# Kernel tuning notes

Measured on AMD Instinct MI355X. Metric: run time of the kernel, lower is better.

Reference implementation:

```python
import jax, jax.numpy as jnp
import numpy as np

EMBED_DIM = 256
NUM_HEADS = 8
HEAD_DIM = EMBED_DIM // NUM_HEADS


def setup_inputs() -> dict:
    key = jax.random.key(0)
    ks = jax.random.split(key, 6)
    B, Nq, Nkv, C = 2, 4096, 4096, EMBED_DIM
    s = 0.02
    return {
        "query": jax.random.normal(ks[0], (B, Nq, C), dtype=jnp.float32),
        "key_value": jax.random.normal(ks[1], (B, Nkv, C), dtype=jnp.float32),
        "w_q": jax.random.normal(ks[2], (C, C), dtype=jnp.float32) * s,
        "w_kv": jax.random.normal(ks[3], (C, 2 * C), dtype=jnp.float32) * s,
        "w_out": jax.random.normal(ks[4], (C, C), dtype=jnp.float32) * s,
        "b_out": jax.random.normal(ks[5], (C,), dtype=jnp.float32) * s,
    }


def reference(query, key_value, w_q, w_kv, w_out, b_out):
    B, Nq, C = query.shape
    Nkv = key_value.shape[1]
    H, D = NUM_HEADS, HEAD_DIM
    scale = D ** -0.5
    # projections (Linear with no bias for q/kv)
    q = (query @ w_q).reshape(B, Nq, H, D).transpose(0, 2, 1, 3)       # [B,H,Nq,D]
    kv = (key_value @ w_kv).reshape(B, Nkv, 2, H, D)
    kv = kv.transpose(2, 0, 3, 1, 4)                                    # [2,B,H,Nkv,D]
    k, v = kv[0], kv[1]
    # full score matrix, as in the original (dropout = eval-mode identity)
    attn = jnp.einsum("bhqd,bhkd->bhqk", q, k) * scale                  # [B,H,Nq,Nkv]
    attn = jax.nn.softmax(attn, axis=-1)
    out = jnp.einsum("bhqk,bhkd->bhqd", attn, v)                        # [B,H,Nq,D]
    out = out.transpose(0, 2, 1, 3).reshape(B, Nq, C)
    return out @ w_out + b_out
```

## Files before the change

kernel.cpp:

```cpp
#include <hip/hip_runtime.h>

typedef __attribute__((ext_vector_type(8))) short bf16x8;
typedef __attribute__((ext_vector_type(4))) float f32x4;
typedef __attribute__((ext_vector_type(16))) float f32x16;

#define NQ   4096
#define NKV  4096
#define CDIM 256
#define HEADS 8
#define DDIM 32
#define APAD 264

__device__ __forceinline__ unsigned short f2bf(float x){
  unsigned int u = __builtin_bit_cast(unsigned int, x);
  u = (u + 0x7FFFu + ((u >> 16) & 1u)) >> 16;
  return (unsigned short)u;
}

__device__ __forceinline__ float bf2f_lo(unsigned int u){
  return __builtin_bit_cast(float, u << 16);
}
__device__ __forceinline__ float bf2f_hi(unsigned int u){
  return __builtin_bit_cast(float, u & 0xFFFF0000u);
}

__global__ __launch_bounds__(256) void prep_w(
    const float* __restrict__ wq, const float* __restrict__ wkv,
    const float* __restrict__ wout,
    unsigned short* __restrict__ wqT, unsigned short* __restrict__ wkvT,
    unsigned short* __restrict__ woutT)
{
  int i = blockIdx.x * 256 + threadIdx.x;
  if (i < 65536){ int n = i >> 8, k = i & 255; wqT[i] = f2bf(wq[k*256 + n]); }
  else if (i < 196608){ int j = i - 65536; int n = j >> 8, k = j & 255;
                        wkvT[j] = f2bf(wkv[k*512 + n]); }
  else { int j = i - 196608; int n = j >> 8, k = j & 255;
         woutT[j] = f2bf(wout[k*256 + n]); }
}

__global__ __launch_bounds__(256) void gemm_qkv(
    const float* __restrict__ qf,
    const float* __restrict__ kvf,
    const unsigned short* __restrict__ wqT,
    const unsigned short* __restrict__ wkvT,
    unsigned short* __restrict__ QT,
    unsigned short* __restrict__ Kb,
    unsigned short* __restrict__ VTb)
{
  __shared__ unsigned short alds[64 * APAD];
  const int tid = threadIdx.x;
  const int wid = tid >> 6;
  const int lane = tid & 63;
  const int l15 = lane & 15, g = lane >> 4;
  const int m0 = blockIdx.x * 64;
  const int mode = blockIdx.y >= 4;
  const int ny = mode ? (blockIdx.y - 4) : blockIdx.y;
  const int n0 = ny * 64 + wid * 16;
  const float* Xf = mode ? kvf : qf;
  const unsigned short* WT = mode ? wkvT : wqT;

  #pragma unroll
  for (int it = 0; it < 8; ++it){
    int c = it * 256 + tid;
    int row = c >> 5, col = (c & 31) * 8;
    const float4* src = (const float4*)(Xf + (size_t)(m0 + row) * CDIM + col);
    float4 a = src[0], b = src[1];
    union { unsigned short u[8]; bf16x8 v; } o;
    o.u[0]=f2bf(a.x); o.u[1]=f2bf(a.y); o.u[2]=f2bf(a.z); o.u[3]=f2bf(a.w);
    o.u[4]=f2bf(b.x); o.u[5]=f2bf(b.y); o.u[6]=f2bf(b.z); o.u[7]=f2bf(b.w);
    *(bf16x8*)(&alds[row * APAD + col]) = o.v;
  }
  __syncthreads();

  f32x4 acc[4] = {{0,0,0,0},{0,0,0,0},{0,0,0,0},{0,0,0,0}};
  const unsigned short* wp = WT + (size_t)(n0 + l15) * CDIM + g * 8;
  #pragma unroll
  for (int k0 = 0; k0 < CDIM; k0 += 32){
    bf16x8 bfr = *(const bf16x8*)(wp + k0);
    #pragma unroll
    for (int i = 0; i < 4; ++i){
      bf16x8 afr = *(const bf16x8*)(&alds[(l15 + i*16) * APAD + k0 + g*8]);
      acc[i] = __builtin_amdgcn_mfma_f32_16x16x32_bf16(afr, bfr, acc[i], 0, 0, 0);
    }
  }
  const int n = n0 + l15;
  const int b = m0 >> 12;
  const int pos0b = (m0 & 4095) + g * 4;
  if (!mode){
    const int h = n >> 5, d = n & 31;
    const size_t rowbase = ((size_t)(b*HEADS + h)*DDIM + d) * NQ;
    #pragma unroll
    for (int i = 0; i < 4; ++i){
      unsigned int p0 = f2bf(acc[i][0] * 0.25503227f);
      unsigned int p1 = f2bf(acc[i][1] * 0.25503227f);
      unsigned int p2 = f2bf(acc[i][2] * 0.25503227f);
      unsigned int p3 = f2bf(acc[i][3] * 0.25503227f);
      *(uint2*)(&QT[rowbase + pos0b + i*16]) = make_uint2(p0 | (p1<<16), p2 | (p3<<16));
    }
  } else if (n < 256){
    const int h = n >> 5, d = n & 31;
    #pragma unroll
    for (int i = 0; i < 4; ++i){
      #pragma unroll
      for (int r = 0; r < 4; ++r){
        Kb[((size_t)(b*HEADS + h)*NKV + (pos0b + i*16 + r))*DDIM + d] = f2bf(acc[i][r]);
      }
    }
  } else {
    const int c = n - 256, h = c >> 5, d = c & 31;
    const size_t rowbase = ((size_t)(b*HEADS + h)*DDIM + d) * NKV;
    #pragma unroll
    for (int i = 0; i < 4; ++i){
      unsigned int p0 = f2bf(acc[i][0]);
      unsigned int p1 = f2bf(acc[i][1]);
      unsigned int p2 = f2bf(acc[i][2]);
      unsigned int p3 = f2bf(acc[i][3]);
      *(uint2*)(&VTb[rowbase + pos0b + i*16]) = make_uint2(p0 | (p1<<16), p2 | (p3<<16));
    }
  }
}

__global__ __launch_bounds__(256) void gemm_out(
    const unsigned short* __restrict__ AO2,
    const unsigned short* __restrict__ WT,
    float* __restrict__ FO,
    const float* __restrict__ bias)
{
  const int wid = threadIdx.x >> 6;
  const int lane = threadIdx.x & 63;
  const int l15 = lane & 15, g = lane >> 4;
  const int m0 = blockIdx.x * 64;
  const int n0 = blockIdx.y * 64 + wid * 16;
  const int base_b = m0 >> 12, pos0 = m0 & 4095;
  f32x4 acc[4] = {{0,0,0,0},{0,0,0,0},{0,0,0,0},{0,0,0,0}};
  const unsigned short* wp = WT + (size_t)(n0 + l15) * CDIM + g * 8;
  #pragma unroll
  for (int k0 = 0; k0 < CDIM; k0 += 32){
    bf16x8 bfr = *(const bf16x8*)(wp + k0);
    const int h = k0 >> 5;
    const unsigned short* xp = AO2
        + ((size_t)(base_b*HEADS + h)*NQ + pos0 + l15)*DDIM + g*8;
    #pragma unroll
    for (int i = 0; i < 4; ++i){
      bf16x8 afr = *(const bf16x8*)(xp + (size_t)i*16*DDIM);
      acc[i] = __builtin_amdgcn_mfma_f32_16x16x32_bf16(afr, bfr, acc[i], 0, 0, 0);
    }
  }
  #pragma unroll
  for (int i = 0; i < 4; ++i){
    #pragma unroll
    for (int r = 0; r < 4; ++r){
      int m = m0 + i*16 + g*4 + r;
      int n = n0 + l15;
      FO[(size_t)m*CDIM + n] = acc[i][r] + bias[n];
    }
  }
}

template<int NSPLIT>
__global__ __launch_bounds__(512, 4) void attn15(
    const unsigned short* __restrict__ QT,
    const unsigned short* __restrict__ Kb,
    const unsigned short* __restrict__ VT,
    unsigned short* __restrict__ P0, unsigned short* __restrict__ P1,
    unsigned short* __restrict__ P2, unsigned short* __restrict__ P3,
    float* __restrict__ ml)
{
  constexpr int NPHASE = 4096 / NSPLIT / 64;
  __shared__ unsigned short lk[4][2048];
  __shared__ unsigned short lv[4][2048];
  const int wid = threadIdx.x >> 6;
  const int lane = threadIdx.x & 63;
  const int l31 = lane & 31, g1 = lane >> 5;
  const int lin = blockIdx.x;
  const int xcd = lin & 7;
  const int j = lin >> 3;
  const int qg = j & 15;
  const int rest = j >> 4;
  const int kvpart = rest & (NSPLIT - 1);
  const int bh = xcd + 8 * (rest / NSPLIT);
  const int q0w = qg * 256 + wid * 32;
  const int kvoff = kvpart * (NPHASE * 64);

  const unsigned short* QTp = QT + (size_t)bh * DDIM * NQ;
  const unsigned short* KpH = Kb + ((size_t)bh * NKV + kvoff) * DDIM;
  const unsigned short* VpH = VT + (size_t)bh * DDIM * NKV + kvoff;

  union { unsigned short u[8]; bf16x8 v; } qa, qb;
  #pragma unroll
  for (int d = 0; d < 8; ++d)
    qa.u[d] = QTp[(size_t)(8*g1 + d) * NQ + q0w + l31];
  #pragma unroll
  for (int d = 0; d < 8; ++d)
    qb.u[d] = QTp[(size_t)(16 + 8*g1 + d) * NQ + q0w + l31];
  const bf16x8 qf0 = qa.v, qf1 = qb.v;

  union { unsigned short u[8]; bf16x8 v; } ones;
  #pragma unroll
  for (int jj = 0; jj < 8; ++jj) ones.u[jj] = 0x3F80;

  const unsigned short* gsrc;
  int gstep, cofs;
  unsigned short* larr;
  if (wid < 4){
    gsrc = KpH + (size_t)((wid >= 2 ? 32 : 0) + l31) * DDIM + 16*(wid & 1) + 8*g1;
    gstep = 64 * DDIM; larr = &lk[0][0]; cofs = wid * 512;
  } else {
    gsrc = VpH + (size_t)l31 * NKV + 16*(wid - 4) + 8*g1;
    gstep = 64; larr = &lv[0][0]; cofs = (wid - 4) * 512;
  }

  f32x16 acc, lac, zero16;
  #pragma unroll
  for (int jj = 0; jj < 16; ++jj){ acc[jj] = 0.0f; lac[jj] = 0.0f; zero16[jj] = 0.0f; }

  __builtin_amdgcn_global_load_lds((const unsigned int*)gsrc,
      (unsigned int*)(larr + cofs), 16, 0, 0);
  gsrc += gstep;
  __builtin_amdgcn_global_load_lds((const unsigned int*)gsrc,
      (unsigned int*)(larr + 2048 + cofs), 16, 0, 0);
  gsrc += gstep;

  int cur = 0, nxt = 2;
  for (int t = 0; t < NPHASE; ++t){
    const bool more = (t + 2) < NPHASE;
    const int dst = more ? nxt : 3;
    __builtin_amdgcn_global_load_lds((const unsigned int*)gsrc,
        (unsigned int*)(larr + dst * 2048 + cofs), 16, 0, 0);
    if (more) gsrc += gstep;
    __builtin_amdgcn_sched_barrier(0);
    asm volatile("s_waitcnt vmcnt(2)" ::: "memory");
    __builtin_amdgcn_s_barrier();
    __builtin_amdgcn_sched_barrier(0);

    bf16x8 kf0 = *(const bf16x8*)(&lk[cur][lane*8]);
    bf16x8 kf1 = *(const bf16x8*)(&lk[cur][512 + lane*8]);
    bf16x8 kf2 = *(const bf16x8*)(&lk[cur][1024 + lane*8]);
    bf16x8 kf3 = *(const bf16x8*)(&lk[cur][1536 + lane*8]);
    bf16x8 vf0 = *(const bf16x8*)(&lv[cur][lane*8]);
    bf16x8 vf1 = *(const bf16x8*)(&lv[cur][512 + lane*8]);
    bf16x8 vf2 = *(const bf16x8*)(&lv[cur][1024 + lane*8]);
    bf16x8 vf3 = *(const bf16x8*)(&lv[cur][1536 + lane*8]);

    __builtin_amdgcn_s_setprio(1);
    f32x16 sa = __builtin_amdgcn_mfma_f32_32x32x16_bf16(kf0, qf0, zero16, 0, 0, 0);
    sa = __builtin_amdgcn_mfma_f32_32x32x16_bf16(kf1, qf1, sa, 0, 0, 0);
    f32x16 sb = __builtin_amdgcn_mfma_f32_32x32x16_bf16(kf2, qf0, zero16, 0, 0, 0);
    sb = __builtin_amdgcn_mfma_f32_32x32x16_bf16(kf3, qf1, sb, 0, 0, 0);
    __builtin_amdgcn_s_setprio(0);

    #pragma unroll
    for (int jj = 0; jj < 16; ++jj) sa[jj] = __builtin_amdgcn_exp2f(sa[jj]);
    #pragma unroll
    for (int jj = 0; jj < 16; ++jj) sb[jj] = __builtin_amdgcn_exp2f(sb[jj]);

    unsigned int a0,a1,a2,a3,a4,a5,a6,a7, b0,b1,b2,b3,b4,b5,b6,b7;
    asm("v_cvt_pk_bf16_f32 %0, %1, %2" : "=v"(a0) : "v"(sa[0]),  "v"(sa[1]));
    asm("v_cvt_pk_bf16_f32 %0, %1, %2" : "=v"(a1) : "v"(sa[2]),  "v"(sa[3]));
    asm("v_cvt_pk_bf16_f32 %0, %1, %2" : "=v"(a2) : "v"(sa[4]),  "v"(sa[5]));
    asm("v_cvt_pk_bf16_f32 %0, %1, %2" : "=v"(a3) : "v"(sa[6]),  "v"(sa[7]));
    asm("v_cvt_pk_bf16_f32 %0, %1, %2" : "=v"(a4) : "v"(sa[8]),  "v"(sa[9]));
    asm("v_cvt_pk_bf16_f32 %0, %1, %2" : "=v"(a5) : "v"(sa[10]), "v"(sa[11]));
    asm("v_cvt_pk_bf16_f32 %0, %1, %2" : "=v"(a6) : "v"(sa[12]), "v"(sa[13]));
    asm("v_cvt_pk_bf16_f32 %0, %1, %2" : "=v"(a7) : "v"(sa[14]), "v"(sa[15]));
    asm("v_permlane32_swap_b32 %0, %1" : "+v"(a0), "+v"(a2));
    asm("v_permlane32_swap_b32 %0, %1" : "+v"(a1), "+v"(a3));
    asm("v_permlane32_swap_b32 %0, %1" : "+v"(a4), "+v"(a6));
    asm("v_permlane32_swap_b32 %0, %1" : "+v"(a5), "+v"(a7));
    asm("v_cvt_pk_bf16_f32 %0, %1, %2" : "=v"(b0) : "v"(sb[0]),  "v"(sb[1]));
    asm("v_cvt_pk_bf16_f32 %0, %1, %2" : "=v"(b1) : "v"(sb[2]),  "v"(sb[3]));
    asm("v_cvt_pk_bf16_f32 %0, %1, %2" : "=v"(b2) : "v"(sb[4]),  "v"(sb[5]));
    asm("v_cvt_pk_bf16_f32 %0, %1, %2" : "=v"(b3) : "v"(sb[6]),  "v"(sb[7]));
    asm("v_cvt_pk_bf16_f32 %0, %1, %2" : "=v"(b4) : "v"(sb[8]),  "v"(sb[9]));
    asm("v_cvt_pk_bf16_f32 %0, %1, %2" : "=v"(b5) : "v"(sb[10]), "v"(sb[11]));
    asm("v_cvt_pk_bf16_f32 %0, %1, %2" : "=v"(b6) : "v"(sb[12]), "v"(sb[13]));
    asm("v_cvt_pk_bf16_f32 %0, %1, %2" : "=v"(b7) : "v"(sb[14]), "v"(sb[15]));
    asm("v_permlane32_swap_b32 %0, %1" : "+v"(b0), "+v"(b2));
    asm("v_permlane32_swap_b32 %0, %1" : "+v"(b1), "+v"(b3));
    asm("v_permlane32_swap_b32 %0, %1" : "+v"(b4), "+v"(b6));
    asm("v_permlane32_swap_b32 %0, %1" : "+v"(b5), "+v"(b7));
    union { unsigned int u[4]; bf16x8 v; } fa0, fa1, fb0, fb1;
    fa0.u[0]=a0; fa0.u[1]=a1; fa0.u[2]=a2; fa0.u[3]=a3;
    fa1.u[0]=a4; fa1.u[1]=a5; fa1.u[2]=a6; fa1.u[3]=a7;
    fb0.u[0]=b0; fb0.u[1]=b1; fb0.u[2]=b2; fb0.u[3]=b3;
    fb1.u[0]=b4; fb1.u[1]=b5; fb1.u[2]=b6; fb1.u[3]=b7;

    __builtin_amdgcn_s_setprio(1);
    acc = __builtin_amdgcn_mfma_f32_32x32x16_bf16(vf0, fa0.v, acc, 0, 0, 0);
    acc = __builtin_amdgcn_mfma_f32_32x32x16_bf16(vf1, fa1.v, acc, 0, 0, 0);
    acc = __builtin_amdgcn_mfma_f32_32x32x16_bf16(vf2, fb0.v, acc, 0, 0, 0);
    acc = __builtin_amdgcn_mfma_f32_32x32x16_bf16(vf3, fb1.v, acc, 0, 0, 0);
    lac = __builtin_amdgcn_mfma_f32_32x32x16_bf16(ones.v, fa0.v, lac, 0, 0, 0);
    lac = __builtin_amdgcn_mfma_f32_32x32x16_bf16(ones.v, fa1.v, lac, 0, 0, 0);
    lac = __builtin_amdgcn_mfma_f32_32x32x16_bf16(ones.v, fb0.v, lac, 0, 0, 0);
    lac = __builtin_amdgcn_mfma_f32_32x32x16_bf16(ones.v, fb1.v, lac, 0, 0, 0);
    __builtin_amdgcn_s_setprio(0);

    cur = (cur == 2) ? 0 : cur + 1;
    nxt = (nxt == 2) ? 0 : nxt + 1;
  }

  float lsum = lac[0];
  unsigned short* Pp;
  if (NSPLIT == 2) Pp = kvpart ? P1 : P0;
  else { if (kvpart == 0) Pp = P0; else if (kvpart == 1) Pp = P1;
         else if (kvpart == 2) Pp = P2; else Pp = P3; }
  Pp += ((size_t)bh * NQ + q0w + l31) * DDIM;
  #pragma unroll
  for (int u = 0; u < 4; ++u){
    unsigned int w0, w1;
    asm("v_cvt_pk_bf16_f32 %0, %1, %2" : "=v"(w0) : "v"(acc[4*u+0]), "v"(acc[4*u+1]));
    asm("v_cvt_pk_bf16_f32 %0, %1, %2" : "=v"(w1) : "v"(acc[4*u+2]), "v"(acc[4*u+3]));
    *(uint2*)(Pp + 8*u + 4*g1) = make_uint2(w0, w1);
  }
  if (g1 == 0){
    size_t ridx = (size_t)bh * NQ + q0w + l31;
    ml[(size_t)kvpart * (16*NQ) + ridx] = lsum;
  }
}

template<int NP>
__global__ __launch_bounds__(256) void attn_merge(
    const unsigned short* __restrict__ P0, const unsigned short* __restrict__ P1,
    const unsigned short* __restrict__ P2, const unsigned short* __restrict__ P3,
    const float* __restrict__ ml, unsigned short* __restrict__ AO2)
{
  const int t = blockIdx.x * 256 + threadIdx.x;
  const size_t row = (size_t)(t >> 2);
  const int u = t & 3;
  const size_t R = (size_t)16 * NQ;
  const unsigned short* parr[4] = {P0, P1, P2, P3};
  float lsum = 0.0f;
  #pragma unroll
  for (int p = 0; p < NP; ++p) lsum += ml[(size_t)p * R + row];
  const float linv = 1.0f / lsum;
  float o[8] = {0,0,0,0,0,0,0,0};
  #pragma unroll
  for (int p = 0; p < NP; ++p){
    uint4 x = *(const uint4*)(parr[p] + row * DDIM + u * 8);
    o[0] += bf2f_lo(x.x); o[1] += bf2f_hi(x.x);
    o[2] += bf2f_lo(x.y); o[3] += bf2f_hi(x.y);
    o[4] += bf2f_lo(x.z); o[5] += bf2f_hi(x.z);
    o[6] += bf2f_lo(x.w); o[7] += bf2f_hi(x.w);
  }
  unsigned int w[4];
  #pragma unroll
  for (int k = 0; k < 4; ++k){
    float a = o[2*k] * linv, b = o[2*k+1] * linv;
    asm("v_cvt_pk_bf16_f32 %0, %1, %2" : "=v"(w[k]) : "v"(a), "v"(b));
  }
  *(uint4*)(AO2 + row * DDIM + u * 8) = make_uint4(w[0], w[1], w[2], w[3]);
}

extern "C" void kernel_launch(void* const* d_in, const int* in_sizes, int n_in,
                              void* d_out, int out_size, void* d_ws, size_t ws_size,
                              hipStream_t stream)
{
  const float* query     = (const float*)d_in[0];
  const float* key_value = (const float*)d_in[1];
  const float* w_q       = (const float*)d_in[2];
  const float* w_kv      = (const float*)d_in[3];
  const float* w_out     = (const float*)d_in[4];
  const float* b_out     = (const float*)d_in[5];
  float* out = (float*)d_out;
  char* ws = (char*)d_ws;
  unsigned short* P0    = (unsigned short*)(ws + 0);
  unsigned short* P1    = (unsigned short*)(ws + 4194304);
  unsigned short* wqT   = (unsigned short*)(ws + 8388608);
  unsigned short* wkvT  = (unsigned short*)(ws + 8519680);
  unsigned short* woutT = (unsigned short*)(ws + 8781824);
  unsigned short* QT    = (unsigned short*)(ws + 8912896);
  unsigned short* Kb    = (unsigned short*)(ws + 13107200);
  unsigned short* VTb   = (unsigned short*)(ws + 17301504);
  unsigned short* AO2   = QT;

  const int nsplit = (ws_size >= 30932992u) ? 4 : 2;
  unsigned short *P2, *P3;
  float* mlb;
  if (nsplit == 4){
    P2  = (unsigned short*)(ws + 21495808);
    P3  = (unsigned short*)(ws + 25690112);
    mlb = (float*)(ws + 29884416);
  } else {
    P2 = P0; P3 = P1;
    mlb = (float*)(ws + 21495808);
  }

  prep_w<<<1024, 256, 0, stream>>>(w_q, w_kv, w_out, wqT, wkvT, woutT);
  gemm_qkv<<<dim3(128, 12), 256, 0, stream>>>(query, key_value, wqT, wkvT, QT, Kb, VTb);
  if (nsplit == 4){
    attn15<4><<<1024, 512, 0, stream>>>(QT, Kb, VTb, P0, P1, P2, P3, mlb);
    attn_merge<4><<<1024, 256, 0, stream>>>(P0, P1, P2, P3, mlb, AO2);
  } else {
    attn15<2><<<512, 512, 0, stream>>>(QT, Kb, VTb, P0, P1, P2, P3, mlb);
    attn_merge<2><<<1024, 256, 0, stream>>>(P0, P1, P2, P3, mlb, AO2);
  }
  gemm_out<<<dim3(128, 4), 256, 0, stream>>>(AO2, woutT, out, b_out);
}
```

Before: 84.89 us.

## Restructure attention kernel to per-wave K register loads and private V buffers

The attention kernel moves from 512-thread blocks with a block-wide shared K/V triple buffer to 256-thread blocks where each wave loads K directly into registers and stages V in its own double-buffered LDS slice. This drops the s_barrier per iteration and shrinks the KV step to 32 so waves advance independently. Grid size doubles and q-groups shrink to 128 rows. The trade-off is that each wave re-reads K and V from global or L2 itself, where before they were shared across 8 waves, so global traffic and load latency exposure rise.

Result: slower. 128.1 us (+50.8%).

```diff
diff --git a/kernel.cpp b/kernel.cpp
--- a/kernel.cpp
+++ b/kernel.cpp
@@ -157,8 +157,42 @@
   }
 }
 
+#define ATTN17_BODY(CURBUF)                                                            \
+  do {                                                                                 \
+    bf16x8 vf0 = *(const bf16x8*)(&lv[wid][(CURBUF)][lane*8]);                         \
+    bf16x8 vf1 = *(const bf16x8*)(&lv[wid][(CURBUF)][512 + lane*8]);                   \
+    __builtin_amdgcn_s_setprio(1);                                                     \
+    f32x16 sa = __builtin_amdgcn_mfma_f32_32x32x16_bf16(kc0, qf0, zero16, 0, 0, 0);    \
+    sa = __builtin_amdgcn_mfma_f32_32x32x16_bf16(kc1, qf1, sa, 0, 0, 0);               \
+    __builtin_amdgcn_s_setprio(0);                                                     \
+    _Pragma("unroll")                                                                  \
+    for (int jj = 0; jj < 16; ++jj) sa[jj] = __builtin_amdgcn_exp2f(sa[jj]);           \
+    unsigned int a0,a1,a2,a3,a4,a5,a6,a7;                                              \
+    asm("v_cvt_pk_bf16_f32 %0, %1, %2" : "=v"(a0) : "v"(sa[0]),  "v"(sa[1]));          \
+    asm("v_cvt_pk_bf16_f32 %0, %1, %2" : "=v"(a1) : "v"(sa[2]),  "v"(sa[3]));          \
+    asm("v_cvt_pk_bf16_f32 %0, %1, %2" : "=v"(a2) : "v"(sa[4]),  "v"(sa[5]));          \
+    asm("v_cvt_pk_bf16_f32 %0, %1, %2" : "=v"(a3) : "v"(sa[6]),  "v"(sa[7]));          \
+    asm("v_cvt_pk_bf16_f32 %0, %1, %2" : "=v"(a4) : "v"(sa[8]),  "v"(sa[9]));          \
+    asm("v_cvt_pk_bf16_f32 %0, %1, %2" : "=v"(a5) : "v"(sa[10]), "v"(sa[11]));         \
+    asm("v_cvt_pk_bf16_f32 %0, %1, %2" : "=v"(a6) : "v"(sa[12]), "v"(sa[13]));         \
+    asm("v_cvt_pk_bf16_f32 %0, %1, %2" : "=v"(a7) : "v"(sa[14]), "v"(sa[15]));         \
+    asm("v_permlane32_swap_b32 %0, %1" : "+v"(a0), "+v"(a2));                          \
+    asm("v_permlane32_swap_b32 %0, %1" : "+v"(a1), "+v"(a3));                          \
+    asm("v_permlane32_swap_b32 %0, %1" : "+v"(a4), "+v"(a6));                          \
+    asm("v_permlane32_swap_b32 %0, %1" : "+v"(a5), "+v"(a7));                          \
+    union { unsigned int u[4]; bf16x8 v; } fa0, fa1;                                   \
+    fa0.u[0]=a0; fa0.u[1]=a1; fa0.u[2]=a2; fa0.u[3]=a3;                                \
+    fa1.u[0]=a4; fa1.u[1]=a5; fa1.u[2]=a6; fa1.u[3]=a7;                                \
+    __builtin_amdgcn_s_setprio(1);                                                     \
+    acc = __builtin_amdgcn_mfma_f32_32x32x16_bf16(vf0, fa0.v, acc, 0, 0, 0);           \
+    acc = __builtin_amdgcn_mfma_f32_32x32x16_bf16(vf1, fa1.v, acc, 0, 0, 0);           \
+    lac = __builtin_amdgcn_mfma_f32_32x32x16_bf16(ones.v, fa0.v, lac, 0, 0, 0);        \
+    lac = __builtin_amdgcn_mfma_f32_32x32x16_bf16(ones.v, fa1.v, lac, 0, 0, 0);        \
+    __builtin_amdgcn_s_setprio(0);                                                     \
+  } while (0)
+
 template<int NSPLIT>
-__global__ __launch_bounds__(512, 4) void attn15(
+__global__ __launch_bounds__(256, 4) void attn17(
     const unsigned short* __restrict__ QT,
     const unsigned short* __restrict__ Kb,
     const unsigned short* __restrict__ VT,
@@ -166,25 +200,26 @@
     unsigned short* __restrict__ P2, unsigned short* __restrict__ P3,
     float* __restrict__ ml)
 {
-  constexpr int NPHASE = 4096 / NSPLIT / 64;
-  __shared__ unsigned short lk[4][2048];
-  __shared__ unsigned short lv[4][2048];
+  constexpr int NPHASE = 4096 / NSPLIT / 32;
+  __shared__ unsigned short lv[4][2][1024];
   const int wid = threadIdx.x >> 6;
   const int lane = threadIdx.x & 63;
   const int l31 = lane & 31, g1 = lane >> 5;
   const int lin = blockIdx.x;
   const int xcd = lin & 7;
   const int j = lin >> 3;
-  const int qg = j & 15;
-  const int rest = j >> 4;
+  const int qg = j & 31;
+  const int rest = j >> 5;
   const int kvpart = rest & (NSPLIT - 1);
   const int bh = xcd + 8 * (rest / NSPLIT);
-  const int q0w = qg * 256 + wid * 32;
-  const int kvoff = kvpart * (NPHASE * 64);
+  const int q0w = qg * 128 + wid * 32;
+  const int kvoff = kvpart * (NPHASE * 32);
 
   const unsigned short* QTp = QT + (size_t)bh * DDIM * NQ;
-  const unsigned short* KpH = Kb + ((size_t)bh * NKV + kvoff) * DDIM;
-  const unsigned short* VpH = VT + (size_t)bh * DDIM * NKV + kvoff;
+  const unsigned short* gKp = Kb + ((size_t)bh * NKV + kvoff) * DDIM
+                              + (size_t)l31 * DDIM + 8 * g1;
+  const unsigned short* gV  = VT + (size_t)bh * DDIM * NKV
+                              + (size_t)l31 * NKV + kvoff + 8 * g1;
 
   union { unsigned short u[8]; bf16x8 v; } qa, qb;
   #pragma unroll
@@ -199,106 +234,39 @@
   #pragma unroll
   for (int jj = 0; jj < 8; ++jj) ones.u[jj] = 0x3F80;
 
-  const unsigned short* gsrc;
-  int gstep, cofs;
-  unsigned short* larr;
-  if (wid < 4){
-    gsrc = KpH + (size_t)((wid >= 2 ? 32 : 0) + l31) * DDIM + 16*(wid & 1) + 8*g1;
-    gstep = 64 * DDIM; larr = &lk[0][0]; cofs = wid * 512;
-  } else {
-    gsrc = VpH + (size_t)l31 * NKV + 16*(wid - 4) + 8*g1;
-    gstep = 64; larr = &lv[0][0]; cofs = (wid - 4) * 512;
-  }
-
   f32x16 acc, lac, zero16;
   #pragma unroll
   for (int jj = 0; jj < 16; ++jj){ acc[jj] = 0.0f; lac[jj] = 0.0f; zero16[jj] = 0.0f; }
 
-  __builtin_amdgcn_global_load_lds((const unsigned int*)gsrc,
-      (unsigned int*)(larr + cofs), 16, 0, 0);
-  gsrc += gstep;
-  __builtin_amdgcn_global_load_lds((const unsigned int*)gsrc,
-      (unsigned int*)(larr + 2048 + cofs), 16, 0, 0);
-  gsrc += gstep;
-
-  int cur = 0, nxt = 2;
-  for (int t = 0; t < NPHASE; ++t){
-    const bool more = (t + 2) < NPHASE;
-    const int dst = more ? nxt : 3;
-    __builtin_amdgcn_global_load_lds((const unsigned int*)gsrc,
-        (unsigned int*)(larr + dst * 2048 + cofs), 16, 0, 0);
-    if (more) gsrc += gstep;
+  __builtin_amdgcn_global_load_lds((const unsigned int*)gV,
+      (unsigned int*)(&lv[wid][0][0]), 16, 0, 0);
+  __builtin_amdgcn_global_load_lds((const unsigned int*)(gV + 16),
+      (unsigned int*)(&lv[wid][0][512]), 16, 0, 0);
+  gV += 32;
+  bf16x8 kc0 = *(const bf16x8*)(gKp);
+  bf16x8 kc1 = *(const bf16x8*)(gKp + 16);
+  gKp += 32 * DDIM;
+
+  #pragma unroll 2
+  for (int t = 0; t < NPHASE - 1; ++t){
+    const int nb = (t + 1) & 1;
+    __builtin_amdgcn_global_load_lds((const unsigned int*)gV,
+        (unsigned int*)(&lv[wid][nb][0]), 16, 0, 0);
+    __builtin_amdgcn_global_load_lds((const unsigned int*)(gV + 16),
+        (unsigned int*)(&lv[wid][nb][512]), 16, 0, 0);
+    gV += 32;
+    bf16x8 kn0 = *(const bf16x8*)(gKp);
+    bf16x8 kn1 = *(const bf16x8*)(gKp + 16);
+    gKp += 32 * DDIM;
     __builtin_amdgcn_sched_barrier(0);
-    asm volatile("s_waitcnt vmcnt(2)" ::: "memory");
-    __builtin_amdgcn_s_barrier();
+    asm volatile("s_waitcnt vmcnt(4)" ::: "memory");
     __builtin_amdgcn_sched_barrier(0);
-
-    bf16x8 kf0 = *(const bf16x8*)(&lk[cur][lane*8]);
-    bf16x8 kf1 = *(const bf16x8*)(&lk[cur][512 + lane*8]);
-    bf16x8 kf2 = *(const bf16x8*)(&lk[cur][1024 + lane*8]);
-    bf16x8 kf3 = *(const bf16x8*)(&lk[cur][1536 + lane*8]);
-    bf16x8 vf0 = *(const bf16x8*)(&lv[cur][lane*8]);
-    bf16x8 vf1 = *(const bf16x8*)(&lv[cur][512 + lane*8]);
-    bf16x8 vf2 = *(const bf16x8*)(&lv[cur][1024 + lane*8]);
-    bf16x8 vf3 = *(const bf16x8*)(&lv[cur][1536 + lane*8]);
-
-    __builtin_amdgcn_s_setprio(1);
-    f32x16 sa = __builtin_amdgcn_mfma_f32_32x32x16_bf16(kf0, qf0, zero16, 0, 0, 0);
-    sa = __builtin_amdgcn_mfma_f32_32x32x16_bf16(kf1, qf1, sa, 0, 0, 0);
-    f32x16 sb = __builtin_amdgcn_mfma_f32_32x32x16_bf16(kf2, qf0, zero16, 0, 0, 0);
-    sb = __builtin_amdgcn_mfma_f32_32x32x16_bf16(kf3, qf1, sb, 0, 0, 0);
-    __builtin_amdgcn_s_setprio(0);
-
-    #pragma unroll
-    for (int jj = 0; jj < 16; ++jj) sa[jj] = __builtin_amdgcn_exp2f(sa[jj]);
-    #pragma unroll
-    for (int jj = 0; jj < 16; ++jj) sb[jj] = __builtin_amdgcn_exp2f(sb[jj]);
-
-    unsigned int a0,a1,a2,a3,a4,a5,a6,a7, b0,b1,b2,b3,b4,b5,b6,b7;
-    asm("v_cvt_pk_bf16_f32 %0, %1, %2" : "=v"(a0) : "v"(sa[0]),  "v"(sa[1]));
-    asm("v_cvt_pk_bf16_f32 %0, %1, %2" : "=v"(a1) : "v"(sa[2]),  "v"(sa[3]));
-    asm("v_cvt_pk_bf16_f32 %0, %1, %2" : "=v"(a2) : "v"(sa[4]),  "v"(sa[5]));
-    asm("v_cvt_pk_bf16_f32 %0, %1, %2" : "=v"(a3) : "v"(sa[6]),  "v"(sa[7]));
-    asm("v_cvt_pk_bf16_f32 %0, %1, %2" : "=v"(a4) : "v"(sa[8]),  "v"(sa[9]));
-    asm("v_cvt_pk_bf16_f32 %0, %1, %2" : "=v"(a5) : "v"(sa[10]), "v"(sa[11]));
-    asm("v_cvt_pk_bf16_f32 %0, %1, %2" : "=v"(a6) : "v"(sa[12]), "v"(sa[13]));
-    asm("v_cvt_pk_bf16_f32 %0, %1, %2" : "=v"(a7) : "v"(sa[14]), "v"(sa[15]));
-    asm("v_permlane32_swap_b32 %0, %1" : "+v"(a0), "+v"(a2));
-    asm("v_permlane32_swap_b32 %0, %1" : "+v"(a1), "+v"(a3));
-    asm("v_permlane32_swap_b32 %0, %1" : "+v"(a4), "+v"(a6));
-    asm("v_permlane32_swap_b32 %0, %1" : "+v"(a5), "+v"(a7));
-    asm("v_cvt_pk_bf16_f32 %0, %1, %2" : "=v"(b0) : "v"(sb[0]),  "v"(sb[1]));
-    asm("v_cvt_pk_bf16_f32 %0, %1, %2" : "=v"(b1) : "v"(sb[2]),  "v"(sb[3]));
-    asm("v_cvt_pk_bf16_f32 %0, %1, %2" : "=v"(b2) : "v"(sb[4]),  "v"(sb[5]));
-    asm("v_cvt_pk_bf16_f32 %0, %1, %2" : "=v"(b3) : "v"(sb[6]),  "v"(sb[7]));
-    asm("v_cvt_pk_bf16_f32 %0, %1, %2" : "=v"(b4) : "v"(sb[8]),  "v"(sb[9]));
-    asm("v_cvt_pk_bf16_f32 %0, %1, %2" : "=v"(b5) : "v"(sb[10]), "v"(sb[11]));
-    asm("v_cvt_pk_bf16_f32 %0, %1, %2" : "=v"(b6) : "v"(sb[12]), "v"(sb[13]));
-    asm("v_cvt_pk_bf16_f32 %0, %1, %2" : "=v"(b7) : "v"(sb[14]), "v"(sb[15]));
-    asm("v_permlane32_swap_b32 %0, %1" : "+v"(b0), "+v"(b2));
-    asm("v_permlane32_swap_b32 %0, %1" : "+v"(b1), "+v"(b3));
-    asm("v_permlane32_swap_b32 %0, %1" : "+v"(b4), "+v"(b6));
-    asm("v_permlane32_swap_b32 %0, %1" : "+v"(b5), "+v"(b7));
-    union { unsigned int u[4]; bf16x8 v; } fa0, fa1, fb0, fb1;
-    fa0.u[0]=a0; fa0.u[1]=a1; fa0.u[2]=a2; fa0.u[3]=a3;
-    fa1.u[0]=a4; fa1.u[1]=a5; fa1.u[2]=a6; fa1.u[3]=a7;
-    fb0.u[0]=b0; fb0.u[1]=b1; fb0.u[2]=b2; fb0.u[3]=b3;
-    fb1.u[0]=b4; fb1.u[1]=b5; fb1.u[2]=b6; fb1.u[3]=b7;
-
-    __builtin_amdgcn_s_setprio(1);
-    acc = __builtin_amdgcn_mfma_f32_32x32x16_bf16(vf0, fa0.v, acc, 0, 0, 0);
-    acc = __builtin_amdgcn_mfma_f32_32x32x16_bf16(vf1, fa1.v, acc, 0, 0, 0);
-    acc = __builtin_amdgcn_mfma_f32_32x32x16_bf16(vf2, fb0.v, acc, 0, 0, 0);
-    acc = __builtin_amdgcn_mfma_f32_32x32x16_bf16(vf3, fb1.v, acc, 0, 0, 0);
-    lac = __builtin_amdgcn_mfma_f32_32x32x16_bf16(ones.v, fa0.v, lac, 0, 0, 0);
-    lac = __builtin_amdgcn_mfma_f32_32x32x16_bf16(ones.v, fa1.v, lac, 0, 0, 0);
-    lac = __builtin_amdgcn_mfma_f32_32x32x16_bf16(ones.v, fb0.v, lac, 0, 0, 0);
-    lac = __builtin_amdgcn_mfma_f32_32x32x16_bf16(ones.v, fb1.v, lac, 0, 0, 0);
-    __builtin_amdgcn_s_setprio(0);
-
-    cur = (cur == 2) ? 0 : cur + 1;
-    nxt = (nxt == 2) ? 0 : nxt + 1;
-  }
+    ATTN17_BODY(t & 1);
+    kc0 = kn0; kc1 = kn1;
+  }
+  asm volatile("s_waitcnt vmcnt(0)" ::: "memory");
+  __builtin_amdgcn_sched_barrier(0);
+  ATTN17_BODY((NPHASE - 1) & 1);
 
   float lsum = lac[0];
   unsigned short* Pp;
@@ -389,10 +357,10 @@
   prep_w<<<1024, 256, 0, stream>>>(w_q, w_kv, w_out, wqT, wkvT, woutT);
   gemm_qkv<<<dim3(128, 12), 256, 0, stream>>>(query, key_value, wqT, wkvT, QT, Kb, VTb);
   if (nsplit == 4){
-    attn15<4><<<1024, 512, 0, stream>>>(QT, Kb, VTb, P0, P1, P2, P3, mlb);
+    attn17<4><<<2048, 256, 0, stream>>>(QT, Kb, VTb, P0, P1, P2, P3, mlb);
     attn_merge<4><<<1024, 256, 0, stream>>>(P0, P1, P2, P3, mlb, AO2);
   } else {
-    attn15<2><<<512, 512, 0, stream>>>(QT, Kb, VTb, P0, P1, P2, P3, mlb);
+    attn17<2><<<1024, 256, 0, stream>>>(QT, Kb, VTb, P0, P1, P2, P3, mlb);
     attn_merge<2><<<1024, 256, 0, stream>>>(P0, P1, P2, P3, mlb, AO2);
   }
   gemm_out<<<dim3(128, 4), 256, 0, stream>>>(AO2, woutT, out, b_out);
```

## Fuse split-KV merge into output projection GEMM via shared memory

Applied to the files above, without the earlier changes.

Removes the separate attn_merge kernel and the intermediate AO2 buffer. Each block of the new output GEMM merges the partial attention outputs for 32 query rows, normalises them by the summed softmax denominators, stages the bf16 tile in LDS, and then runs the MFMA projection with bias. This saves a kernel launch and a global write and read of the merged activations. In exchange it uses a smaller grid of 256 blocks and recomputes the merge per block.

Measured after the change: 79.48 us. -6.4%, faster.

```diff
diff --git a/kernel.cpp b/kernel.cpp
--- a/kernel.cpp
+++ b/kernel.cpp
@@ -116,43 +116,6 @@
       unsigned int p2 = f2bf(acc[i][2]);
       unsigned int p3 = f2bf(acc[i][3]);
       *(uint2*)(&VTb[rowbase + pos0b + i*16]) = make_uint2(p0 | (p1<<16), p2 | (p3<<16));
-    }
-  }
-}
-
-__global__ __launch_bounds__(256) void gemm_out(
-    const unsigned short* __restrict__ AO2,
-    const unsigned short* __restrict__ WT,
-    float* __restrict__ FO,
-    const float* __restrict__ bias)
-{
-  const int wid = threadIdx.x >> 6;
-  const int lane = threadIdx.x & 63;
-  const int l15 = lane & 15, g = lane >> 4;
-  const int m0 = blockIdx.x * 64;
-  const int n0 = blockIdx.y * 64 + wid * 16;
-  const int base_b = m0 >> 12, pos0 = m0 & 4095;
-  f32x4 acc[4] = {{0,0,0,0},{0,0,0,0},{0,0,0,0},{0,0,0,0}};
-  const unsigned short* wp = WT + (size_t)(n0 + l15) * CDIM + g * 8;
-  #pragma unroll
-  for (int k0 = 0; k0 < CDIM; k0 += 32){
-    bf16x8 bfr = *(const bf16x8*)(wp + k0);
-    const int h = k0 >> 5;
-    const unsigned short* xp = AO2
-        + ((size_t)(base_b*HEADS + h)*NQ + pos0 + l15)*DDIM + g*8;
-    #pragma unroll
-    for (int i = 0; i < 4; ++i){
-      bf16x8 afr = *(const bf16x8*)(xp + (size_t)i*16*DDIM);
-      acc[i] = __builtin_amdgcn_mfma_f32_16x16x32_bf16(afr, bfr, acc[i], 0, 0, 0);
-    }
-  }
-  #pragma unroll
-  for (int i = 0; i < 4; ++i){
-    #pragma unroll
-    for (int r = 0; r < 4; ++r){
-      int m = m0 + i*16 + g*4 + r;
-      int n = n0 + l15;
-      FO[(size_t)m*CDIM + n] = acc[i][r] + bias[n];
     }
   }
 }
@@ -320,36 +283,83 @@
 }
 
 template<int NP>
-__global__ __launch_bounds__(256) void attn_merge(
+__global__ __launch_bounds__(512) void gemm_out2(
     const unsigned short* __restrict__ P0, const unsigned short* __restrict__ P1,
     const unsigned short* __restrict__ P2, const unsigned short* __restrict__ P3,
-    const float* __restrict__ ml, unsigned short* __restrict__ AO2)
+    const float* __restrict__ ml,
+    const unsigned short* __restrict__ WT,
+    float* __restrict__ FO,
+    const float* __restrict__ bias)
 {
-  const int t = blockIdx.x * 256 + threadIdx.x;
-  const size_t row = (size_t)(t >> 2);
-  const int u = t & 3;
+  __shared__ unsigned short alds[32 * APAD];
+  const int tid = threadIdx.x;
+  const int m0 = blockIdx.x * 32;
+  const int b = m0 >> 12;
+  const int pos0 = m0 & 4095;
   const size_t R = (size_t)16 * NQ;
   const unsigned short* parr[4] = {P0, P1, P2, P3};
-  float lsum = 0.0f;
-  #pragma unroll
-  for (int p = 0; p < NP; ++p) lsum += ml[(size_t)p * R + row];
-  const float linv = 1.0f / lsum;
-  float o[8] = {0,0,0,0,0,0,0,0};
-  #pragma unroll
-  for (int p = 0; p < NP; ++p){
-    uint4 x = *(const uint4*)(parr[p] + row * DDIM + u * 8);
-    o[0] += bf2f_lo(x.x); o[1] += bf2f_hi(x.x);
-    o[2] += bf2f_lo(x.y); o[3] += bf2f_hi(x.y);
-    o[4] += bf2f_lo(x.z); o[5] += bf2f_hi(x.z);
-    o[6] += bf2f_lo(x.w); o[7] += bf2f_hi(x.w);
-  }
-  unsigned int w[4];
-  #pragma unroll
-  for (int k = 0; k < 4; ++k){
-    float a = o[2*k] * linv, b = o[2*k+1] * linv;
-    asm("v_cvt_pk_bf16_f32 %0, %1, %2" : "=v"(w[k]) : "v"(a), "v"(b));
-  }
-  *(uint4*)(AO2 + row * DDIM + u * 8) = make_uint4(w[0], w[1], w[2], w[3]);
+
+  #pragma unroll
+  for (int it = 0; it < 2; ++it){
+    int G = it * 512 + tid;
+    int row = G >> 5, col8 = G & 31;
+    int col = col8 * 8;
+    int h = col8 >> 2, dcol = (col8 & 3) * 8;
+    size_t ridx = (size_t)(b*HEADS + h) * NQ + pos0 + row;
+    float lsum = 0.0f;
+    #pragma unroll
+    for (int p = 0; p < NP; ++p) lsum += ml[(size_t)p * R + ridx];
+    float linv = 1.0f / lsum;
+    float o[8] = {0,0,0,0,0,0,0,0};
+    #pragma unroll
+    for (int p = 0; p < NP; ++p){
+      uint4 x = *(const uint4*)(parr[p] + ridx * DDIM + dcol);
+      o[0] += bf2f_lo(x.x); o[1] += bf2f_hi(x.x);
+      o[2] += bf2f_lo(x.y); o[3] += bf2f_hi(x.y);
+      o[4] += bf2f_lo(x.z); o[5] += bf2f_hi(x.z);
+      o[6] += bf2f_lo(x.w); o[7] += bf2f_hi(x.w);
+    }
+    unsigned int w[4];
+    #pragma unroll
+    for (int k = 0; k < 4; ++k){
+      float a = o[2*k] * linv, bb = o[2*k+1] * linv;
+      asm("v_cvt_pk_bf16_f32 %0, %1, %2" : "=v"(w[k]) : "v"(a), "v"(bb));
+    }
+    *(uint4*)(&alds[row * APAD + col]) = make_uint4(w[0], w[1], w[2], w[3]);
+  }
+  __syncthreads();
+
+  const int wid = tid >> 6;
+  const int lane = tid & 63;
+  const int l15 = lane & 15, g = lane >> 4;
+  const int n0 = wid * 32;
+  f32x4 acc[2][2] = {{{0,0,0,0},{0,0,0,0}},{{0,0,0,0},{0,0,0,0}}};
+  const unsigned short* wp0 = WT + (size_t)(n0 + l15) * CDIM + g * 8;
+  const unsigned short* wp1 = WT + (size_t)(n0 + 16 + l15) * CDIM + g * 8;
+  #pragma unroll
+  for (int k0 = 0; k0 < CDIM; k0 += 32){
+    bf16x8 bfr0 = *(const bf16x8*)(wp0 + k0);
+    bf16x8 bfr1 = *(const bf16x8*)(wp1 + k0);
+    bf16x8 afr0 = *(const bf16x8*)(&alds[(l15) * APAD + k0 + g*8]);
+    bf16x8 afr1 = *(const bf16x8*)(&alds[(l15 + 16) * APAD + k0 + g*8]);
+    acc[0][0] = __builtin_amdgcn_mfma_f32_16x16x32_bf16(afr0, bfr0, acc[0][0], 0, 0, 0);
+    acc[0][1] = __builtin_amdgcn_mfma_f32_16x16x32_bf16(afr0, bfr1, acc[0][1], 0, 0, 0);
+    acc[1][0] = __builtin_amdgcn_mfma_f32_16x16x32_bf16(afr1, bfr0, acc[1][0], 0, 0, 0);
+    acc[1][1] = __builtin_amdgcn_mfma_f32_16x16x32_bf16(afr1, bfr1, acc[1][1], 0, 0, 0);
+  }
+  #pragma unroll
+  for (int i = 0; i < 2; ++i){
+    #pragma unroll
+    for (int jj = 0; jj < 2; ++jj){
+      int n = n0 + jj*16 + l15;
+      float bv = bias[n];
+      #pragma unroll
+      for (int r = 0; r < 4; ++r){
+        int m = m0 + i*16 + g*4 + r;
+        FO[(size_t)m * CDIM + n] = acc[i][jj][r] + bv;
+      }
+    }
+  }
 }
 
 extern "C" void kernel_launch(void* const* d_in, const int* in_sizes, int n_in,
@@ -372,7 +382,6 @@
   unsigned short* QT    = (unsigned short*)(ws + 8912896);
   unsigned short* Kb    = (unsigned short*)(ws + 13107200);
   unsigned short* VTb   = (unsigned short*)(ws + 17301504);
-  unsigned short* AO2   = QT;
 
   const int nsplit = (ws_size >= 30932992u) ? 4 : 2;
   unsigned short *P2, *P3;
@@ -390,10 +399,9 @@
   gemm_qkv<<<dim3(128, 12), 256, 0, stream>>>(query, key_value, wqT, wkvT, QT, Kb, VTb);
   if (nsplit == 4){
     attn15<4><<<1024, 512, 0, stream>>>(QT, Kb, VTb, P0, P1, P2, P3, mlb);
-    attn_merge<4><<<1024, 256, 0, stream>>>(P0, P1, P2, P3, mlb, AO2);
+    gemm_out2<4><<<256, 512, 0, stream>>>(P0, P1, P2, P3, mlb, woutT, out, b_out);
   } else {
     attn15<2><<<512, 512, 0, stream>>>(QT, Kb, VTb, P0, P1, P2, P3, mlb);
-    attn_merge<2><<<1024, 256, 0, stream>>>(P0, P1, P2, P3, mlb, AO2);
-  }
-  gemm_out<<<dim3(128, 4), 256, 0, stream>>>(AO2, woutT, out, b_out);
-}
+    gemm_out2<2><<<256, 512, 0, stream>>>(P0, P1, P2, P3, mlb, woutT, out, b_out);
+  }
+}
```
